# Performance work log

Hardware: AMD Instinct MI355X
Metric: run time of the kernel (lower is better)

Reference implementation:

```python
import jax, jax.numpy as jnp
import numpy as np

B, NO, O, H = 8, 512, 1024, 16  # batch, num_obj(=max_len=max_len_k), output_size, heads
DH = O // H
SCALE = 1.0 / (DH ** 0.5)
NEG = -1e9


def setup_inputs() -> dict:
    key = jax.random.key(0)
    ks = jax.random.split(key, 16)
    std = 0.02
    inp = {
        "v": jax.random.normal(ks[0], (B, NO, O), jnp.float32),
        "q": jax.random.normal(ks[1], (B, NO, O), jnp.float32),
        "k": jax.random.normal(ks[2], (B, NO, O), jnp.float32),
        "v_mask": jax.random.randint(ks[3], (B, NO), 0, 2, jnp.int32),
        "q_mask": jax.random.randint(ks[4], (B, NO), 0, 2, jnp.int32),
        "k_mask": jax.random.randint(ks[5], (B, NO), 0, 2, jnp.int32),
        # projection weights (stored as [in, out] so x @ W + b)
        "Wv": jax.random.normal(ks[6], (O, 3 * O), jnp.float32) * std,
        "bv": jnp.zeros((3 * O,), jnp.float32),
        "Wq": jax.random.normal(ks[7], (O, 3 * O), jnp.float32) * std,
        "bq": jnp.zeros((3 * O,), jnp.float32),
        "Wk": jax.random.normal(ks[8], (O, 3 * O), jnp.float32) * std,
        "bk": jnp.zeros((3 * O,), jnp.float32),
        "Wvo": jax.random.normal(ks[9], (O + O, O), jnp.float32) * std,   # v_output: [output+v_size, output]
        "bvo": jnp.zeros((O,), jnp.float32),
        "Wko": jax.random.normal(ks[10], (O + O + O, O), jnp.float32) * std,  # k_output: [output+k_size+v_size, output]
        "bko": jnp.zeros((O,), jnp.float32),
    }
    return inp


def _heads(x):
    # [B, L, O] -> [B, L, H, DH]
    b, l, _ = x.shape
    return x.reshape(b, l, H, DH)


def _attn(qh, kh, vh, mask):
    # qh,kh,vh: [B, L, H, DH]; mask: [B, Lk] (0/1)
    s = jnp.einsum('bnhd,bmhd->bhnm', qh, kh)
    # torch applies masked_fill THEN divides by sqrt(dh): replicate exactly
    s = jnp.where(mask[:, None, None, :] == 0, NEG, s) * SCALE
    a = jax.nn.softmax(s, axis=-1)
    out = jnp.einsum('bhnm,bmhd->bnhd', a, vh)
    return out.reshape(out.shape[0], out.shape[1], O)


def reference(v, q, k, v_mask, q_mask, k_mask, Wv, bv, Wq, bq, Wk, bk, Wvo, bvo, Wko, bko):
    vm = v_mask.astype(v.dtype)[:, :, None]
    qm = q_mask.astype(q.dtype)[:, :, None]
    km = k_mask.astype(k.dtype)[:, :, None]

    v_tr = (jax.nn.relu(v) @ Wv + bv) * vm
    q_tr = (jax.nn.relu(q) @ Wq + bq) * qm
    k_tr = (jax.nn.relu(k) @ Wk + bk) * km

    v_k, v_q, v_v = jnp.split(v_tr, 3, axis=2)
    q_k, q_q, q_v = jnp.split(q_tr, 3, axis=2)
    k_k, k_q, k_v = jnp.split(k_tr, 3, axis=2)

    # faithful to source bug: kv_set is split from k_q (values for k2v are k_q)
    vq_update = _attn(_heads(v_q), _heads(q_k), _heads(q_v), q_mask)  # q->v
    vk_update = _attn(_heads(k_q), _heads(k_k), _heads(k_q), k_mask)  # k self, values = k_q

    updated_v = jnp.concatenate([v, vq_update], axis=2) @ Wvo + bvo
    updated_V = jnp.concatenate([v, vq_update, vk_update], axis=2) @ Wko + bko
    return updated_V, updated_v
```

## Files before the change

### kernel.cpp

```cpp
#include <hip/hip_runtime.h>


typedef float  f32x4  __attribute__((ext_vector_type(4)));
typedef short  bf16x8 __attribute__((ext_vector_type(8)));
typedef unsigned short u16;
typedef unsigned short u16x8v __attribute__((ext_vector_type(8)));

constexpr float ATT_SCALE = 0.125f;
constexpr float NEGS      = -1.25e8f;

#define MiB (size_t(1) << 20)
constexpr size_t O_VR_H = 0*MiB,  O_VR_L = 8*MiB;
constexpr size_t O_QR_H = 16*MiB, O_QR_L = 24*MiB;
constexpr size_t O_KR_H = 32*MiB, O_KR_L = 40*MiB;
constexpr size_t O_WP   = 48*MiB;
constexpr size_t O_PO   = 68*MiB;
constexpr size_t O_VT0  = 0*MiB,  O_VT1 = 8*MiB;
constexpr size_t O_OVQ_H= 16*MiB, O_OVQ_L= 24*MiB;
constexpr size_t O_OVK_H= 32*MiB, O_OVK_L= 40*MiB;
constexpr size_t O_V2_H = 48*MiB, O_V2_L = 56*MiB;
constexpr size_t O_WVO_H= 64*MiB, O_WVO_L= 68*MiB;
constexpr size_t O_WKO_H= 72*MiB, O_WKO_L= 78*MiB;

__device__ __forceinline__ u16 f2bf_rne(float x) {
  unsigned u = __float_as_uint(x);
  return (u16)((u + 0x7FFFu + ((u >> 16) & 1u)) >> 16);
}
__device__ __forceinline__ float bf2f(u16 h) {
  return __uint_as_float(((unsigned)h) << 16);
}
__device__ __forceinline__ void gload16(const void* g, void* l) {
  __builtin_amdgcn_global_load_lds(
      (const __attribute__((address_space(1))) unsigned int*)g,
      (__attribute__((address_space(3))) unsigned int*)l, 16, 0, 0);
}

__global__ __launch_bounds__(256) void prep_act(
    const float* __restrict__ s0, const float* __restrict__ s1, const float* __restrict__ s2,
    char* __restrict__ ws, const int relu,
    const size_t o0h, const size_t o0l, const size_t o1h, const size_t o1l,
    const size_t o2h, const size_t o2l)
{
  const int z = blockIdx.z;
  const float* src = (z == 0) ? s0 : (z == 1) ? s1 : s2;
  u16* dh = (u16*)(ws + ((z == 0) ? o0h : (z == 1) ? o1h : o2h));
  u16* dl = (u16*)(ws + ((z == 0) ? o0l : (z == 1) ? o1l : o2l));
  const int idx = blockIdx.x * 256 + threadIdx.x;
  const int r = idx & 127, kg = (idx >> 7) & 3, kt = (idx >> 9) & 31, rt = idx >> 14;
  const float* p = src + (size_t)(rt * 128 + r) * 1024 + kt * 32 + kg * 8;
  const float4 x0 = ((const float4*)p)[0];
  const float4 x1 = ((const float4*)p)[1];
  const float xv[8] = {x0.x, x0.y, x0.z, x0.w, x1.x, x1.y, x1.z, x1.w};
  u16x8v hv, lv;
#pragma unroll
  for (int e = 0; e < 8; ++e) {
    const float x = relu ? fmaxf(xv[e], 0.f) : xv[e];
    const u16 hi = f2bf_rne(x);
    hv[e] = hi;
    lv[e] = f2bf_rne(x - bf2f(hi));
  }
  *(u16x8v*)(dh + (size_t)idx * 8) = hv;
  *(u16x8v*)(dl + (size_t)idx * 8) = lv;
}

__global__ __launch_bounds__(256) void prep_w(
    const float* __restrict__ W0, const float* __restrict__ W1, const float* __restrict__ W2,
    char* __restrict__ ws, const int mode)
{
  __shared__ float T[32][129];
  const int kt = blockIdx.x, ntile = blockIdx.y, z = blockIdx.z;
  const float* src; int ld, c0, nkt; u16 *dh, *dl;
  if (mode == 0) {
    const int c0s[5] = {1024, 0, 2048, 0, 1024};
    src = (z == 0) ? W0 : (z <= 2) ? W1 : W2;
    ld = 3072; c0 = c0s[z]; nkt = 32;
    dh = (u16*)(ws + O_WP + (size_t)z * 4 * MiB);
    dl = (u16*)(ws + O_WP + (size_t)z * 4 * MiB + 2 * MiB);
  } else if (mode == 1) {
    src = W0; ld = 1024; c0 = 0; nkt = 64;
    dh = (u16*)(ws + O_WVO_H); dl = (u16*)(ws + O_WVO_L);
  } else {
    src = W0; ld = 1024; c0 = 0; nkt = 96;
    dh = (u16*)(ws + O_WKO_H); dl = (u16*)(ws + O_WKO_L);
  }
  const int tid = threadIdx.x;
#pragma unroll
  for (int j = 0; j < 4; ++j) {
    const int p = tid + j * 256;
    const int row = p >> 5, c4 = p & 31;
    const float4 v = *(const float4*)(src + (size_t)(kt * 32 + row) * ld + c0 + ntile * 128 + c4 * 4);
    T[row][c4 * 4 + 0] = v.x; T[row][c4 * 4 + 1] = v.y;
    T[row][c4 * 4 + 2] = v.z; T[row][c4 * 4 + 3] = v.w;
  }
  __syncthreads();
#pragma unroll
  for (int j = 0; j < 2; ++j) {
    const int c = tid + j * 256;
    const int kg = c >> 7, rr = c & 127;
    u16x8v hv, lv;
#pragma unroll
    for (int e = 0; e < 8; ++e) {
      const float x = T[kg * 8 + e][rr];
      const u16 hi = f2bf_rne(x);
      hv[e] = hi;
      lv[e] = f2bf_rne(x - bf2f(hi));
    }
    const size_t off = (size_t)(ntile * nkt + kt) * 4096 + (size_t)c * 8;
    *(u16x8v*)(dh + off) = hv;
    *(u16x8v*)(dl + off) = lv;
  }
}

__device__ __forceinline__ void sgemm_core(
    const u16* __restrict__ a0h, const u16* __restrict__ a0l,
    const u16* __restrict__ a1h, const u16* __restrict__ a1l,
    const u16* __restrict__ a2h, const u16* __restrict__ a2l,
    const u16* __restrict__ bh,  const u16* __restrict__ bl,
    const int nkt, const int mt, const int nt, f32x4 acc[4][4])
{
  __shared__ __align__(16) u16 lds[4][4096];
  const int tid = threadIdx.x;
  const int wid = tid >> 6, lane = tid & 63;
  const int lr = lane & 15, lg = lane >> 4;
  const int wm = (wid >> 1) * 64, wn = (wid & 1) * 64;
  u16* myl = &lds[wid][0];

  for (int kt = 0; kt < nkt; ++kt) {
    __syncthreads();
    const int p = kt >> 5, kk = kt & 31;
    const u16* ah = (p == 0) ? a0h : (p == 1) ? a1h : a2h;
    const u16* al = (p == 0) ? a0l : (p == 1) ? a1l : a2l;
    const u16* src;
    if      (wid == 0) src = ah + (size_t)(mt * 32 + kk) * 4096;
    else if (wid == 1) src = al + (size_t)(mt * 32 + kk) * 4096;
    else if (wid == 2) src = bh + (size_t)(nt * nkt + kt) * 4096;
    else               src = bl + (size_t)(nt * nkt + kt) * 4096;
    const u16* s = src + lane * 8;
#pragma unroll
    for (int i = 0; i < 8; ++i)
      gload16(s + i * 512, myl + i * 512);
    __syncthreads();

    bf16x8 afh[4], afl[4], bfh[4], bfl[4];
#pragma unroll
    for (int i = 0; i < 4; ++i) {
      const int ra = wm + i * 16 + lr;
      const int rb = wn + i * 16 + lr;
      afh[i] = *(const bf16x8*)&lds[0][(lg * 128 + ra) * 8];
      afl[i] = *(const bf16x8*)&lds[1][(lg * 128 + ra) * 8];
      bfh[i] = *(const bf16x8*)&lds[2][(lg * 128 + rb) * 8];
      bfl[i] = *(const bf16x8*)&lds[3][(lg * 128 + rb) * 8];
    }
#pragma unroll
    for (int i = 0; i < 4; ++i)
#pragma unroll
      for (int j = 0; j < 4; ++j) {
        acc[i][j] = __builtin_amdgcn_mfma_f32_16x16x32_bf16(afh[i], bfh[j], acc[i][j], 0, 0, 0);
        acc[i][j] = __builtin_amdgcn_mfma_f32_16x16x32_bf16(afh[i], bfl[j], acc[i][j], 0, 0, 0);
        acc[i][j] = __builtin_amdgcn_mfma_f32_16x16x32_bf16(afl[i], bfh[j], acc[i][j], 0, 0, 0);
      }
  }
}

__global__ __launch_bounds__(256) void proj_gemm(
    char* __restrict__ ws,
    const float* __restrict__ bv, const float* __restrict__ bq, const float* __restrict__ bk,
    const int* __restrict__ vm, const int* __restrict__ qm, const int* __restrict__ km)
{
  const int z = blockIdx.z, nt = blockIdx.x, mt = blockIdx.y;
  const u16* ah = (const u16*)(ws + ((z == 0) ? O_VR_H : (z <= 2) ? O_QR_H : O_KR_H));
  const u16* al = (const u16*)(ws + ((z == 0) ? O_VR_L : (z <= 2) ? O_QR_L : O_KR_L));
  const u16* bh = (const u16*)(ws + O_WP + (size_t)z * 4 * MiB);
  const u16* bl = (const u16*)(ws + O_WP + (size_t)z * 4 * MiB + 2 * MiB);
  const float* bias = (z == 0) ? bv + 1024 : (z == 1) ? bq : (z == 2) ? bq + 2048
                    : (z == 3) ? bk : bk + 1024;
  const int* msk = (z == 0) ? vm : (z <= 2) ? qm : km;
  u16* out = (u16*)(ws + O_PO + (size_t)z * 8 * MiB);

  f32x4 acc[4][4];
#pragma unroll
  for (int i = 0; i < 4; ++i)
#pragma unroll
    for (int j = 0; j < 4; ++j) {
      f32x4 zer = {0.f, 0.f, 0.f, 0.f};
      acc[i][j] = zer;
    }
  sgemm_core(ah, al, ah, al, ah, al, bh, bl, 32, mt, nt, acc);

  const int tid = threadIdx.x, wid = tid >> 6, lane = tid & 63;
  const int lr = lane & 15, lg = lane >> 4;
  const int row0 = mt * 128 + (wid >> 1) * 64;
  const int col0 = nt * 128 + (wid & 1) * 64;
#pragma unroll
  for (int i = 0; i < 4; ++i)
#pragma unroll
    for (int r = 0; r < 4; ++r) {
      const int row = row0 + i * 16 + lg * 4 + r;
      const float mf = (float)msk[row];
#pragma unroll
      for (int j = 0; j < 4; ++j) {
        const int col = col0 + j * 16 + lr;
        out[(size_t)row * 1024 + col] = f2bf_rne((acc[i][j][r] + bias[col]) * mf);
      }
    }
}

__global__ __launch_bounds__(256) void transpose_vt(char* __restrict__ ws) {
  const int z = blockIdx.z, bh = blockIdx.y, kb = blockIdx.x;
  const u16* src = (const u16*)(ws + O_PO + (size_t)((z == 0) ? 2 : 4) * 8 * MiB);
  u16* dst = (u16*)(ws + ((z == 0) ? O_VT0 : O_VT1));
  __shared__ __align__(16) u16 T[64][80];
  const int tid = threadIdx.x;
  const int b = bh >> 4, h = bh & 15;
#pragma unroll
  for (int j = 0; j < 2; ++j) {
    const int p = tid + j * 256;
    const int row = p >> 3, sl = p & 7;
    const u16x8v val = *(const u16x8v*)(src + (size_t)(b * 512 + kb * 64 + row) * 1024 + h * 64 + sl * 8);
    *(u16x8v*)&T[row][sl * 8] = val;
  }
  __syncthreads();
#pragma unroll
  for (int j = 0; j < 2; ++j) {
    const int p = tid + j * 256;
    const int d = p >> 3, ks = p & 7;
    u16x8v val;
#pragma unroll
    for (int e = 0; e < 8; ++e) val[e] = T[ks * 8 + e][d];
    *(u16x8v*)(dst + (size_t)(bh * 64 + d) * 512 + kb * 64 + ks * 8) = val;
  }
}

__global__ __launch_bounds__(256) void attn_kernel(
    char* __restrict__ ws, const int* __restrict__ qm, const int* __restrict__ km)
{
  __shared__ __align__(16) u16 Qs[4096], Ks[4096], Vs[4096];
  __shared__ __align__(16) float Ps[4][16 * 68];
  __shared__ int msk[64];
  const int z = blockIdx.z, b = z >> 1, att = z & 1;
  const int h = blockIdx.y, q0 = blockIdx.x * 64;
  const u16 *Qg, *Kg, *VTg; const int* mg; u16 *Ohp, *Olp;
  if (att == 0) {
    Qg  = (const u16*)(ws + O_PO + 0 * 8 * MiB);
    Kg  = (const u16*)(ws + O_PO + 1 * 8 * MiB);
    VTg = (const u16*)(ws + O_VT0);
    mg = qm; Ohp = (u16*)(ws + O_OVQ_H); Olp = (u16*)(ws + O_OVQ_L);
  } else {
    Qg  = (const u16*)(ws + O_PO + 4 * 8 * MiB);
    Kg  = (const u16*)(ws + O_PO + 3 * 8 * MiB);
    VTg = (const u16*)(ws + O_VT1);
    mg = km; Ohp = (u16*)(ws + O_OVK_H); Olp = (u16*)(ws + O_OVK_L);
  }
  const int tid = threadIdx.x, wid = tid >> 6, lane = tid & 63;
  const int lr = lane & 15, lg = lane >> 4;

#pragma unroll
  for (int i = 0; i < 2; ++i) {
    const int p = wid * 128 + i * 64 + lane;
    const int row = p >> 3, sl = p & 7;
    const u16* src = Qg + (size_t)(b * 512 + q0 + row) * 1024 + h * 64 + ((sl ^ (row & 7)) * 8);
    gload16(src, &Qs[(wid * 128 + i * 64) * 8]);
  }
  __syncthreads();
  const int qrow = wid * 16 + lr;
  const bf16x8 qa0 = *(const bf16x8*)&Qs[(qrow * 8 + ((0 + lg) ^ (qrow & 7))) * 8];
  const bf16x8 qa1 = *(const bf16x8*)&Qs[(qrow * 8 + ((4 + lg) ^ (qrow & 7))) * 8];

  f32x4 oacc[4];
  float mreg[4], lreg[4];
#pragma unroll
  for (int i = 0; i < 4; ++i) {
    f32x4 zer = {0.f, 0.f, 0.f, 0.f};
    oacc[i] = zer; mreg[i] = -3.0e38f; lreg[i] = 0.f;
  }

  for (int kt = 0; kt < 8; ++kt) {
    __syncthreads();
#pragma unroll
    for (int i = 0; i < 2; ++i) {
      const int p = wid * 128 + i * 64 + lane;
      const int row = p >> 3, sl = p & 7;
      const u16* ksrc = Kg + (size_t)(b * 512 + kt * 64 + row) * 1024 + h * 64 + ((sl ^ (row & 7)) * 8);
      gload16(ksrc, &Ks[(wid * 128 + i * 64) * 8]);
      const u16* vsrc = VTg + (size_t)((b * 16 + h) * 64 + row) * 512 + kt * 64 + ((sl ^ (row & 7)) * 8);
      gload16(vsrc, &Vs[(wid * 128 + i * 64) * 8]);
    }
    if (tid < 64) msk[tid] = mg[b * 512 + kt * 64 + tid];
    __syncthreads();

    f32x4 s[4];
#pragma unroll
    for (int nt = 0; nt < 4; ++nt) {
      f32x4 zer = {0.f, 0.f, 0.f, 0.f};
      s[nt] = zer;
      const int kr = nt * 16 + lr;
      const bf16x8 kb0 = *(const bf16x8*)&Ks[(kr * 8 + ((0 + lg) ^ (kr & 7))) * 8];
      const bf16x8 kb1 = *(const bf16x8*)&Ks[(kr * 8 + ((4 + lg) ^ (kr & 7))) * 8];
      s[nt] = __builtin_amdgcn_mfma_f32_16x16x32_bf16(qa0, kb0, s[nt], 0, 0, 0);
      s[nt] = __builtin_amdgcn_mfma_f32_16x16x32_bf16(qa1, kb1, s[nt], 0, 0, 0);
    }
#pragma unroll
    for (int nt = 0; nt < 4; ++nt) {
      const int mk = msk[nt * 16 + lr];
#pragma unroll
      for (int r = 0; r < 4; ++r)
        s[nt][r] = mk ? s[nt][r] * ATT_SCALE : NEGS;
    }
#pragma unroll
    for (int r = 0; r < 4; ++r) {
      float mx = fmaxf(fmaxf(s[0][r], s[1][r]), fmaxf(s[2][r], s[3][r]));
      mx = fmaxf(mx, __shfl_xor(mx, 1)); mx = fmaxf(mx, __shfl_xor(mx, 2));
      mx = fmaxf(mx, __shfl_xor(mx, 4)); mx = fmaxf(mx, __shfl_xor(mx, 8));
      const float nm = fmaxf(mreg[r], mx);
      const float corr = __expf(mreg[r] - nm);
      float ps = 0.f;
#pragma unroll
      for (int nt = 0; nt < 4; ++nt) {
        const float pv = __expf(s[nt][r] - nm);
        s[nt][r] = pv; ps += pv;
      }
      ps += __shfl_xor(ps, 1); ps += __shfl_xor(ps, 2);
      ps += __shfl_xor(ps, 4); ps += __shfl_xor(ps, 8);
      lreg[r] = lreg[r] * corr + ps;
      mreg[r] = nm;
#pragma unroll
      for (int d = 0; d < 4; ++d) oacc[d][r] *= corr;
    }
    float* Pw = &Ps[wid][0];
#pragma unroll
    for (int nt = 0; nt < 4; ++nt)
#pragma unroll
      for (int r = 0; r < 4; ++r)
        Pw[(lg * 4 + r) * 68 + nt * 16 + lr] = s[nt][r];
#pragma unroll
    for (int ks = 0; ks < 2; ++ks) {
      const float* pp = &Pw[lr * 68 + ks * 32 + lg * 8];
      const f32x4 p0 = *(const f32x4*)pp;
      const f32x4 p1 = *(const f32x4*)(pp + 4);
      bf16x8 pa;
      pa[0] = (short)f2bf_rne(p0[0]); pa[1] = (short)f2bf_rne(p0[1]);
      pa[2] = (short)f2bf_rne(p0[2]); pa[3] = (short)f2bf_rne(p0[3]);
      pa[4] = (short)f2bf_rne(p1[0]); pa[5] = (short)f2bf_rne(p1[1]);
      pa[6] = (short)f2bf_rne(p1[2]); pa[7] = (short)f2bf_rne(p1[3]);
#pragma unroll
      for (int d = 0; d < 4; ++d) {
        const int vr = d * 16 + lr;
        const bf16x8 vb = *(const bf16x8*)&Vs[(vr * 8 + ((ks * 4 + lg) ^ (vr & 7))) * 8];
        oacc[d] = __builtin_amdgcn_mfma_f32_16x16x32_bf16(pa, vb, oacc[d], 0, 0, 0);
      }
    }
  }

#pragma unroll
  for (int r = 0; r < 4; ++r) {
    const float inv = 1.0f / lreg[r];
    const int row = b * 512 + q0 + wid * 16 + lg * 4 + r;
    const int rt = row >> 7, rr = row & 127;
#pragma unroll
    for (int d = 0; d < 4; ++d) {
      const int col = h * 64 + d * 16 + lr;
      const int ktc = col >> 5, kg = (col >> 3) & 3, e = col & 7;
      const size_t off = ((((size_t)rt * 32 + ktc) * 4 + kg) * 128 + rr) * 8 + e;
      const float x = oacc[d][r] * inv;
      const u16 hi = f2bf_rne(x);
      Ohp[off] = hi;
      Olp[off] = f2bf_rne(x - bf2f(hi));
    }
  }
}

__global__ __launch_bounds__(256) void out_gemm(
    char* __restrict__ ws, const float* __restrict__ bvo, const float* __restrict__ bko,
    float* __restrict__ dout)
{
  const int z = blockIdx.z, nt = blockIdx.x, mt = blockIdx.y;
  const u16* a0h = (const u16*)(ws + O_V2_H);
  const u16* a0l = (const u16*)(ws + O_V2_L);
  const u16* a1h = (const u16*)(ws + O_OVQ_H);
  const u16* a1l = (const u16*)(ws + O_OVQ_L);
  const u16* a2h = (const u16*)(ws + O_OVK_H);
  const u16* a2l = (const u16*)(ws + O_OVK_L);
  const int nkt = z ? 96 : 64;
  const u16* bh = (const u16*)(ws + (z ? O_WKO_H : O_WVO_H));
  const u16* bl = (const u16*)(ws + (z ? O_WKO_L : O_WVO_L));
  const float* bias = z ? bko : bvo;
  float* dst = z ? dout : (dout + (size_t)4096 * 1024);

  f32x4 acc[4][4];
#pragma unroll
  for (int i = 0; i < 4; ++i)
#pragma unroll
    for (int j = 0; j < 4; ++j) {
      f32x4 zer = {0.f, 0.f, 0.f, 0.f};
      acc[i][j] = zer;
    }
  sgemm_core(a0h, a0l, a1h, a1l, a2h, a2l, bh, bl, nkt, mt, nt, acc);

  const int tid = threadIdx.x, wid = tid >> 6, lane = tid & 63;
  const int lr = lane & 15, lg = lane >> 4;
  const int row0 = mt * 128 + (wid >> 1) * 64;
  const int col0 = nt * 128 + (wid & 1) * 64;
#pragma unroll
  for (int i = 0; i < 4; ++i)
#pragma unroll
    for (int r = 0; r < 4; ++r) {
      const int row = row0 + i * 16 + lg * 4 + r;
#pragma unroll
      for (int j = 0; j < 4; ++j) {
        const int col = col0 + j * 16 + lr;
        dst[(size_t)row * 1024 + col] = acc[i][j][r] + bias[col];
      }
    }
}

extern "C" void kernel_launch(void* const* d_in, const int* in_sizes, int n_in,
                              void* d_out, int out_size, void* d_ws, size_t ws_size,
                              hipStream_t stream) {
  const float* v  = (const float*)d_in[0];
  const float* q  = (const float*)d_in[1];
  const float* k  = (const float*)d_in[2];
  const int* vm   = (const int*)d_in[3];
  const int* qm   = (const int*)d_in[4];
  const int* km   = (const int*)d_in[5];
  const float* Wv = (const float*)d_in[6];
  const float* bv = (const float*)d_in[7];
  const float* Wq = (const float*)d_in[8];
  const float* bq = (const float*)d_in[9];
  const float* Wk = (const float*)d_in[10];
  const float* bk = (const float*)d_in[11];
  const float* Wvo = (const float*)d_in[12];
  const float* bvo = (const float*)d_in[13];
  const float* Wko = (const float*)d_in[14];
  const float* bko = (const float*)d_in[15];
  char* ws = (char*)d_ws;
  float* out = (float*)d_out;

  prep_act<<<dim3(2048, 1, 3), 256, 0, stream>>>(v, q, k, ws, 1,
      O_VR_H, O_VR_L, O_QR_H, O_QR_L, O_KR_H, O_KR_L);
  prep_w<<<dim3(32, 8, 5), 256, 0, stream>>>(Wv, Wq, Wk, ws, 0);
  proj_gemm<<<dim3(8, 32, 5), 256, 0, stream>>>(ws, bv, bq, bk, vm, qm, km);
  transpose_vt<<<dim3(8, 128, 2), 256, 0, stream>>>(ws);
  attn_kernel<<<dim3(8, 16, 16), 256, 0, stream>>>(ws, qm, km);
  prep_act<<<dim3(2048, 1, 1), 256, 0, stream>>>(v, v, v, ws, 0,
      O_V2_H, O_V2_L, O_V2_H, O_V2_L, O_V2_H, O_V2_L);
  prep_w<<<dim3(64, 8, 1), 256, 0, stream>>>(Wvo, Wvo, Wvo, ws, 1);
  prep_w<<<dim3(96, 8, 1), 256, 0, stream>>>(Wko, Wko, Wko, ws, 2);
  out_gemm<<<dim3(8, 32, 2), 256, 0, stream>>>(ws, bvo, bko, out);
}
```

Measured before the change: 514.5 us.

## Drop weight low-part MFMA in projection GEMM and add XCD-aware block swizzle

```diff
diff --git a/kernel.cpp b/kernel.cpp
--- a/kernel.cpp
+++ b/kernel.cpp
@@ -33,6 +33,10 @@
   __builtin_amdgcn_global_load_lds(
       (const __attribute__((address_space(1))) unsigned int*)g,
       (__attribute__((address_space(3))) unsigned int*)l, 16, 0, 0);
+}
+template <int NWG>
+__device__ __forceinline__ int xcd_swz(int bid) {
+  return (bid & 7) * (NWG >> 3) + (bid >> 3);
 }
 
 __global__ __launch_bounds__(256) void prep_act(
@@ -111,6 +115,7 @@
   }
 }
 
+template <int NM>
 __device__ __forceinline__ void sgemm_core(
     const u16* __restrict__ a0h, const u16* __restrict__ a0l,
     const u16* __restrict__ a1h, const u16* __restrict__ a1l,
@@ -130,15 +135,17 @@
     const int p = kt >> 5, kk = kt & 31;
     const u16* ah = (p == 0) ? a0h : (p == 1) ? a1h : a2h;
     const u16* al = (p == 0) ? a0l : (p == 1) ? a1l : a2l;
-    const u16* src;
+    const u16* src = nullptr;
     if      (wid == 0) src = ah + (size_t)(mt * 32 + kk) * 4096;
     else if (wid == 1) src = al + (size_t)(mt * 32 + kk) * 4096;
     else if (wid == 2) src = bh + (size_t)(nt * nkt + kt) * 4096;
-    else               src = bl + (size_t)(nt * nkt + kt) * 4096;
-    const u16* s = src + lane * 8;
-#pragma unroll
-    for (int i = 0; i < 8; ++i)
-      gload16(s + i * 512, myl + i * 512);
+    else if (NM == 3)  src = bl + (size_t)(nt * nkt + kt) * 4096;
+    if (src) {
+      const u16* s = src + lane * 8;
+#pragma unroll
+      for (int i = 0; i < 8; ++i)
+        gload16(s + i * 512, myl + i * 512);
+    }
     __syncthreads();
 
     bf16x8 afh[4], afl[4], bfh[4], bfl[4];
@@ -149,14 +156,15 @@
       afh[i] = *(const bf16x8*)&lds[0][(lg * 128 + ra) * 8];
       afl[i] = *(const bf16x8*)&lds[1][(lg * 128 + ra) * 8];
       bfh[i] = *(const bf16x8*)&lds[2][(lg * 128 + rb) * 8];
-      bfl[i] = *(const bf16x8*)&lds[3][(lg * 128 + rb) * 8];
+      if (NM == 3) bfl[i] = *(const bf16x8*)&lds[3][(lg * 128 + rb) * 8];
     }
 #pragma unroll
     for (int i = 0; i < 4; ++i)
 #pragma unroll
       for (int j = 0; j < 4; ++j) {
         acc[i][j] = __builtin_amdgcn_mfma_f32_16x16x32_bf16(afh[i], bfh[j], acc[i][j], 0, 0, 0);
-        acc[i][j] = __builtin_amdgcn_mfma_f32_16x16x32_bf16(afh[i], bfl[j], acc[i][j], 0, 0, 0);
+        if (NM == 3)
+          acc[i][j] = __builtin_amdgcn_mfma_f32_16x16x32_bf16(afh[i], bfl[j], acc[i][j], 0, 0, 0);
         acc[i][j] = __builtin_amdgcn_mfma_f32_16x16x32_bf16(afl[i], bfh[j], acc[i][j], 0, 0, 0);
       }
   }
@@ -167,11 +175,13 @@
     const float* __restrict__ bv, const float* __restrict__ bq, const float* __restrict__ bk,
     const int* __restrict__ vm, const int* __restrict__ qm, const int* __restrict__ km)
 {
-  const int z = blockIdx.z, nt = blockIdx.x, mt = blockIdx.y;
+  const int swz = xcd_swz<1280>(blockIdx.x);
+  const int nt = swz & 7, t = swz >> 3;
+  const int mt = t & 31, z = t >> 5;
+
   const u16* ah = (const u16*)(ws + ((z == 0) ? O_VR_H : (z <= 2) ? O_QR_H : O_KR_H));
   const u16* al = (const u16*)(ws + ((z == 0) ? O_VR_L : (z <= 2) ? O_QR_L : O_KR_L));
   const u16* bh = (const u16*)(ws + O_WP + (size_t)z * 4 * MiB);
-  const u16* bl = (const u16*)(ws + O_WP + (size_t)z * 4 * MiB + 2 * MiB);
   const float* bias = (z == 0) ? bv + 1024 : (z == 1) ? bq : (z == 2) ? bq + 2048
                     : (z == 3) ? bk : bk + 1024;
   const int* msk = (z == 0) ? vm : (z <= 2) ? qm : km;
@@ -185,7 +195,7 @@
       f32x4 zer = {0.f, 0.f, 0.f, 0.f};
       acc[i][j] = zer;
     }
-  sgemm_core(ah, al, ah, al, ah, al, bh, bl, 32, mt, nt, acc);
+  sgemm_core<2>(ah, al, ah, al, ah, al, bh, nullptr, 32, mt, nt, acc);
 
   const int tid = threadIdx.x, wid = tid >> 6, lane = tid & 63;
   const int lr = lane & 15, lg = lane >> 4;
@@ -237,8 +247,10 @@
   __shared__ __align__(16) u16 Qs[4096], Ks[4096], Vs[4096];
   __shared__ __align__(16) float Ps[4][16 * 68];
   __shared__ int msk[64];
-  const int z = blockIdx.z, b = z >> 1, att = z & 1;
-  const int h = blockIdx.y, q0 = blockIdx.x * 64;
+  const int swz = xcd_swz<2048>(blockIdx.x);
+  const int qt = swz & 7, h = (swz >> 3) & 15, zz = swz >> 7;
+  const int b = zz >> 1, att = zz & 1;
+  const int q0 = qt * 64;
   const u16 *Qg, *Kg, *VTg; const int* mg; u16 *Ohp, *Olp;
   if (att == 0) {
     Qg  = (const u16*)(ws + O_PO + 0 * 8 * MiB);
@@ -373,7 +385,9 @@
     char* __restrict__ ws, const float* __restrict__ bvo, const float* __restrict__ bko,
     float* __restrict__ dout)
 {
-  const int z = blockIdx.z, nt = blockIdx.x, mt = blockIdx.y;
+  const int swz = xcd_swz<512>(blockIdx.x);
+  const int nt = swz & 7, z = (swz >> 3) & 1, mt = swz >> 4;
+
   const u16* a0h = (const u16*)(ws + O_V2_H);
   const u16* a0l = (const u16*)(ws + O_V2_L);
   const u16* a1h = (const u16*)(ws + O_OVQ_H);
@@ -394,7 +408,7 @@
       f32x4 zer = {0.f, 0.f, 0.f, 0.f};
       acc[i][j] = zer;
     }
-  sgemm_core(a0h, a0l, a1h, a1l, a2h, a2l, bh, bl, nkt, mt, nt, acc);
+  sgemm_core<3>(a0h, a0l, a1h, a1l, a2h, a2l, bh, bl, nkt, mt, nt, acc);
 
   const int tid = threadIdx.x, wid = tid >> 6, lane = tid & 63;
   const int lr = lane & 15, lg = lane >> 4;
@@ -438,12 +452,12 @@
   prep_act<<<dim3(2048, 1, 3), 256, 0, stream>>>(v, q, k, ws, 1,
       O_VR_H, O_VR_L, O_QR_H, O_QR_L, O_KR_H, O_KR_L);
   prep_w<<<dim3(32, 8, 5), 256, 0, stream>>>(Wv, Wq, Wk, ws, 0);
-  proj_gemm<<<dim3(8, 32, 5), 256, 0, stream>>>(ws, bv, bq, bk, vm, qm, km);
+  proj_gemm<<<dim3(1280), 256, 0, stream>>>(ws, bv, bq, bk, vm, qm, km);
   transpose_vt<<<dim3(8, 128, 2), 256, 0, stream>>>(ws);
-  attn_kernel<<<dim3(8, 16, 16), 256, 0, stream>>>(ws, qm, km);
+  attn_kernel<<<dim3(2048), 256, 0, stream>>>(ws, qm, km);
   prep_act<<<dim3(2048, 1, 1), 256, 0, stream>>>(v, v, v, ws, 0,
       O_V2_H, O_V2_L, O_V2_H, O_V2_L, O_V2_H, O_V2_L);
   prep_w<<<dim3(64, 8, 1), 256, 0, stream>>>(Wvo, Wvo, Wvo, ws, 1);
   prep_w<<<dim3(96, 8, 1), 256, 0, stream>>>(Wko, Wko, Wko, ws, 2);
-  out_gemm<<<dim3(8, 32, 2), 256, 0, stream>>>(ws, bvo, bko, out);
-}
+  out_gemm<<<dim3(512), 256, 0, stream>>>(ws, bvo, bko, out);
+}
```

Result: faster. 462.1 us (-10.2%).
